# Kernel optimization log

Hardware: AMD Instinct MI355X
Metric: run time of the kernel (lower is better)

Reference implementation:

```python
import jax, jax.numpy as jnp
import numpy as np

B, S, H, GLU, VOC, L, CIN, BLK = 8, 256, 512, 1024, 256, 24, 320, 16
EPS = 1e-5


def setup_inputs() -> dict:
    key = jax.random.key(0)
    ks = jax.random.split(key, 16)
    r = lambda k, shp, s=0.02: (jax.random.normal(k, shp) * s).astype(jnp.float32)
    return {
        "x": jax.random.normal(ks[0], (B, CIN, 1, S), dtype=jnp.float32),
        "stem_w": r(ks[1], (H, CIN)),
        "rms_local": jnp.ones((L, H), jnp.float32),
        "rms_global": jnp.ones((L, H), jnp.float32),
        "rms_ffn": jnp.ones((L, H), jnp.float32),
        # alphas init to 0.0 in the torch module; use small nonzero values so
        # all sublayers actually contribute to the output / gradients.
        "alpha_local": (jax.random.normal(ks[2], (L,)) * 0.1).astype(jnp.float32),
        "alpha_global": (jax.random.normal(ks[3], (L,)) * 0.1).astype(jnp.float32),
        "alpha_mlp": (jax.random.normal(ks[4], (L,)) * 0.1).astype(jnp.float32),
        "w_local": r(ks[5], (L, H, BLK, BLK), 0.06),   # per-channel 16x16 mixing mats
        "w_global": r(ks[6], (L, H, BLK, BLK), 0.06),
        "wv": r(ks[7], (L, GLU, H)),
        "wg": r(ks[8], (L, GLU, H)),
        "wo": r(ks[9], (L, H, GLU)),
        "head_rms": jnp.ones((H,), jnp.float32),
        "head_logit_scale": jnp.float32(1.0),
        "head_w": r(ks[10], (VOC, H)),
    }


def _rmsnorm(h, w):
    # h: [B,C,S], w: [C]; mean-of-squares over channel axis (C == HIDDEN == 512)
    ms = jnp.mean(h * h, axis=1, keepdims=True)
    return h * jax.lax.rsqrt(ms + EPS) * w[None, :, None]


def _forward(x, stem_w, rms_local, rms_global, rms_ffn, alpha_local, alpha_global,
             alpha_mlp, w_local, w_global, wv, wg, wo, head_rms, head_logit_scale, head_w):
    h = jnp.einsum('oc,bcs->bos', stem_w, x[:, :, 0, :])  # stem conv1x1 -> [B,H,S]
    params = (rms_local, rms_global, rms_ffn, alpha_local, alpha_global, alpha_mlp,
              w_local, w_global, wv, wg, wo)

    def step(h, p):
        rl, rg, rf, al, ag, am, Wl, Wg, Wv, Wgt, Wo = p
        # s = i*16 + j : i = chunk index, j = within-chunk position
        u = _rmsnorm(h, rl).reshape(B, H, BLK, BLK)
        h = h + al * jnp.einsum('cpj,bcij->bcip', Wl, u).reshape(B, H, S)   # local: mix j
        v = _rmsnorm(h, rg).reshape(B, H, BLK, BLK)
        h = h + ag * jnp.einsum('cpi,bcij->bcpj', Wg, v).reshape(B, H, S)   # global: mix i
        w_ = _rmsnorm(h, rf)
        h1 = jnp.einsum('oc,bcs->bos', Wv, w_)
        h3 = jnp.einsum('oc,bcs->bos', Wgt, w_)
        h = h + am * jnp.einsum('co,bos->bcs', Wo, jax.nn.silu(h1) * h3)    # GLU MLP
        return h, None

    h, _ = jax.lax.scan(step, h, params)
    n = _rmsnorm(h, head_rms)
    logits = head_logit_scale * jnp.einsum('vc,bcs->bvs', head_w, n)
    return logits[:, :, None, :]  # [B, VOCAB, 1, S]


def reference(x, stem_w, rms_local, rms_global, rms_ffn, alpha_local, alpha_global,
              alpha_mlp, w_local, w_global, wv, wg, wo, head_rms, head_logit_scale, head_w):
    return _forward(x, stem_w, rms_local, rms_global, rms_ffn, alpha_local, alpha_global,
                    alpha_mlp, w_local, w_global, wv, wg, wo, head_rms,
                    head_logit_scale, head_w)
```

## Files before the change

kernel.cpp:

```cpp
#include <hip/hip_runtime.h>
#include <hip/hip_bf16.h>
#include <stdint.h>

#define NB 8
#define NS 256
#define NH 512
#define NG 1024
#define NV 256
#define NL 24
#define NC 320
#define NT 2048
#define EPSF 1e-5f

typedef __bf16 bf16;
typedef bf16 bf16x8 __attribute__((ext_vector_type(8)));
typedef float f32x4 __attribute__((ext_vector_type(4)));

__device__ __forceinline__ bf16 f2bf(float f) {
    uint32_t u = __builtin_bit_cast(uint32_t, f);
    u += 0x7FFFu + ((u >> 16) & 1u);
    uint16_t b = (uint16_t)(u >> 16);
    return __builtin_bit_cast(bf16, b);
}
__device__ __forceinline__ uint16_t bfbits(float f) {
    uint32_t u = __builtin_bit_cast(uint32_t, f);
    u += 0x7FFFu + ((u >> 16) & 1u);
    return (uint16_t)(u >> 16);
}

__device__ __forceinline__ void gload16(const void* g, void* l) {
    __builtin_amdgcn_global_load_lds(
        (const __attribute__((address_space(1))) void*)g,
        (__attribute__((address_space(3))) void*)l,
        16, 0, 0);
}

__device__ __forceinline__ void stage64(
    const bf16* __restrict__ src, int ldk, bf16* lds, int wv_, int lane)
{
    #pragma unroll
    for (int j = 0; j < 2; ++j) {
        const int gI = wv_*2 + j;
        const int r  = gI*8 + (lane >> 3);
        const int ch = (lane & 7) ^ (lane >> 3);
        gload16(src + (size_t)r*ldk + ch*8, lds + gI*512);
    }
}
__device__ __forceinline__ const bf16x8* fragp(const bf16* lds, int row, int ch) {
    return (const bf16x8*)(lds + row*64 + ((ch ^ (row & 7)) << 3));
}

#define MFMA(a,b,c) __builtin_amdgcn_mfma_f32_16x16x32_bf16(a, b, c, 0, 0, 0)

__global__ __launch_bounds__(256) void k_cvt(
    const float* __restrict__ src, bf16* __restrict__ dst, int n8)
{
    int i = blockIdx.x*256 + threadIdx.x;
    const int stride = gridDim.x*256;
    for (; i < n8; i += stride) {
        const float* sp = src + (size_t)i*8;
        float4 v0 = *(const float4*)&sp[0];
        float4 v1 = *(const float4*)&sp[4];
        bf16x8 t;
        t[0] = f2bf(v0.x); t[1] = f2bf(v0.y); t[2] = f2bf(v0.z); t[3] = f2bf(v0.w);
        t[4] = f2bf(v1.x); t[5] = f2bf(v1.y); t[6] = f2bf(v1.z); t[7] = f2bf(v1.w);
        *(bf16x8*)&dst[(size_t)i*8] = t;
    }
}

__global__ __launch_bounds__(256) void k_cvt2(
    const float* __restrict__ s0, const float* __restrict__ s1,
    bf16* __restrict__ d0, bf16* __restrict__ d1, int n8a, int n8b)
{
    const int N = n8a + n8b;
    for (int i = blockIdx.x*256 + threadIdx.x; i < N; i += gridDim.x*256) {
        const float* s; bf16* d; int j;
        if (i < n8a) { s = s0; d = d0; j = i; }
        else         { s = s1; d = d1; j = i - n8a; }
        const float* sp = s + (size_t)j*8;
        float4 v0 = *(const float4*)&sp[0];
        float4 v1 = *(const float4*)&sp[4];
        bf16x8 t;
        t[0] = f2bf(v0.x); t[1] = f2bf(v0.y); t[2] = f2bf(v0.z); t[3] = f2bf(v0.w);
        t[4] = f2bf(v1.x); t[5] = f2bf(v1.y); t[6] = f2bf(v1.z); t[7] = f2bf(v1.w);
        *(bf16x8*)&d[(size_t)j*8] = t;
    }
}

__global__ __launch_bounds__(256) void k_trw(
    const float* __restrict__ wl, const float* __restrict__ wg,
    bf16* __restrict__ wlT, bf16* __restrict__ wgT)
{
    __shared__ bf16 Ls[64*72];
    const int pj0 = blockIdx.x*64, c0 = blockIdx.y*64;
    const int z = blockIdx.z, l = z >> 1;
    const float* src = (z & 1) ? wg : wl;
    bf16* dst = (z & 1) ? wgT : wlT;
    src += (size_t)l*NH*256;
    dst += (size_t)l*256*NH;
    const int tid = threadIdx.x;
    #pragma unroll
    for (int e = 0; e < 16; ++e) {
        int idx = e*256 + tid;
        int cl = idx >> 6, pj = idx & 63;
        Ls[pj*72 + cl] = f2bf(src[(size_t)(c0 + cl)*256 + pj0 + pj]);
    }
    __syncthreads();
    #pragma unroll
    for (int e = 0; e < 2; ++e) {
        int idx = e*256 + tid;
        int row = idx >> 3, ch8 = idx & 7;
        *(bf16x8*)&dst[(size_t)(pj0 + row)*NH + c0 + ch8*8] =
            *(const bf16x8*)&Ls[row*72 + ch8*8];
    }
}

__global__ __launch_bounds__(256) void k_trx(
    const float* __restrict__ x, bf16* __restrict__ xT)
{
    __shared__ bf16 Ls[64*72];
    const int s0 = blockIdx.x*64, c0 = blockIdx.y*64, b = blockIdx.z;
    const int tid = threadIdx.x;
    #pragma unroll
    for (int e = 0; e < 16; ++e) {
        int idx = tid + e*256;
        int c = idx >> 6, s = idx & 63;
        Ls[s*72 + c] = f2bf(x[(size_t)(b*NC + c0 + c)*NS + s0 + s]);
    }
    __syncthreads();
    #pragma unroll
    for (int e = 0; e < 2; ++e) {
        int idx = tid + e*256;
        int s = idx >> 3, ch = idx & 7;
        *(bf16x8*)&xT[(size_t)(b*NS + s0 + s)*NC + c0 + ch*8] =
            *(const bf16x8*)&Ls[s*72 + ch*8];
    }
}

__global__ __launch_bounds__(256) void k_stem_b(
    const bf16* __restrict__ xT, const bf16* __restrict__ wb,
    float* __restrict__ h)
{
    __shared__ __align__(16) bf16 As[2][4096], Bs[2][4096];
    __shared__ float Cs[64*66];
    const int t0 = blockIdx.x*64, n0 = blockIdx.y*64;
    const int tid = threadIdx.x, lane = tid & 63, wv_ = tid >> 6;
    const int wm = wv_ >> 1, wn = wv_ & 1;
    const int fr = lane & 15, kq = lane >> 4;
    const bf16* Ag = xT + (size_t)t0*NC;
    const bf16* Bg = wb + (size_t)n0*NC;
    f32x4 acc[2][2] = {};
    stage64(Ag, NC, As[0], wv_, lane);
    stage64(Bg, NC, Bs[0], wv_, lane);
    __syncthreads();
    const int NIT = NC/64;
    for (int it = 0; it < NIT; ++it) {
        const int cur = it & 1;
        if (it + 1 < NIT) {
            stage64(Ag + (it+1)*64, NC, As[cur^1], wv_, lane);
            stage64(Bg + (it+1)*64, NC, Bs[cur^1], wv_, lane);
        }
        #pragma unroll
        for (int kk = 0; kk < 2; ++kk) {
            const int ch = kk*4 + kq;
            bf16x8 a0 = *fragp(As[cur], wm*32 + fr,      ch);
            bf16x8 a1 = *fragp(As[cur], wm*32 + 16 + fr, ch);
            bf16x8 b0 = *fragp(Bs[cur], wn*32 + fr,      ch);
            bf16x8 b1 = *fragp(Bs[cur], wn*32 + 16 + fr, ch);
            acc[0][0] = MFMA(a0, b0, acc[0][0]);
            acc[0][1] = MFMA(a0, b1, acc[0][1]);
            acc[1][0] = MFMA(a1, b0, acc[1][0]);
            acc[1][1] = MFMA(a1, b1, acc[1][1]);
        }
        __syncthreads();
    }
    const int row4 = (lane >> 4)*4, col = lane & 15;
    #pragma unroll
    for (int mi = 0; mi < 2; ++mi)
      #pragma unroll
      for (int ni = 0; ni < 2; ++ni)
        #pragma unroll
        for (int r = 0; r < 4; ++r)
            Cs[(wm*32 + mi*16 + row4 + r)*66 + wn*32 + ni*16 + col] = acc[mi][ni][r];
    __syncthreads();
    const int rr = tid >> 2, c16 = (tid & 3)*16;
    float* dst = &h[(size_t)(t0 + rr)*NH + n0 + c16];
    #pragma unroll
    for (int i = 0; i < 16; ++i) dst[i] = Cs[rr*66 + c16 + i];
}

template<int STR, bool FFN>
__global__ __launch_bounds__(256) void k_mix2(
    float* __restrict__ h, const bf16* __restrict__ wT,
    const float* __restrict__ rmsw, const float* __restrict__ alpha_p,
    const float* __restrict__ rmsw_ffn, bf16* __restrict__ a_bf)
{
    __shared__ float raw[16][512];
    __shared__ float red[4][16];
    __shared__ float rstdL[16];
    const int b = blockIdx.x, gi = blockIdx.y, ph = blockIdx.z;
    const int base = b*NS + (STR == 1 ? gi*16 : gi);
    const int tid = threadIdx.x, lane = tid & 63, wid = tid >> 6;
    #pragma unroll
    for (int e = 0; e < 8; ++e) {
        int idx = e*256 + tid;
        int k = idx >> 7, c4 = idx & 127;
        *(float4*)&raw[k][c4*4] = *(const float4*)&h[(size_t)(base + k*STR)*NH + c4*4];
    }
    __syncthreads();
    const int c0 = tid*2;
    float u0[16], u1[16], part[16];
    #pragma unroll
    for (int k = 0; k < 16; ++k) {
        float A = raw[k][c0], B = raw[k][c0+1];
        u0[k] = A; u1[k] = B; part[k] = A*A + B*B;
    }
    #pragma unroll
    for (int m = 1; m < 64; m <<= 1)
        #pragma unroll
        for (int k = 0; k < 16; ++k) part[k] += __shfl_xor(part[k], m, 64);
    if (lane == 0) {
        #pragma unroll
        for (int k = 0; k < 16; ++k) red[wid][k] = part[k];
    }
    __syncthreads();
    if (tid < 16)
        rstdL[tid] = rsqrtf((red[0][tid]+red[1][tid]+red[2][tid]+red[3][tid])*(1.f/NH) + EPSF);
    __syncthreads();
    #pragma unroll
    for (int k = 0; k < 16; ++k) { u0[k] *= rstdL[k]; u1[k] *= rstdL[k]; }
    const float al = *alpha_p;
    const float rc0 = rmsw[c0]*al, rc1 = rmsw[c0+1]*al;
    const uint32_t* wrow = (const uint32_t*)wT + tid;
    float hn0[8], hn1[8];
    #pragma unroll
    for (int pp = 0; pp < 8; ++pp) {
        const int p = ph*8 + pp;
        float a0 = 0.f, a1 = 0.f;
        #pragma unroll
        for (int k = 0; k < 16; ++k) {
            uint32_t wz = wrow[(p*16 + k)*256];
            float w0 = __builtin_bit_cast(float, wz << 16);
            float w1 = __builtin_bit_cast(float, wz & 0xffff0000u);
            a0 += w0*u0[k]; a1 += w1*u1[k];
        }
        hn0[pp] = raw[p][c0]   + rc0*a0;
        hn1[pp] = raw[p][c0+1] + rc1*a1;
        float2 o; o.x = hn0[pp]; o.y = hn1[pp];
        *(float2*)&h[(size_t)(base + p*STR)*NH + c0] = o;
    }
    if constexpr (FFN) {
        float p2[8];
        #pragma unroll
        for (int pp = 0; pp < 8; ++pp) p2[pp] = hn0[pp]*hn0[pp] + hn1[pp]*hn1[pp];
        #pragma unroll
        for (int m = 1; m < 64; m <<= 1)
            #pragma unroll
            for (int pp = 0; pp < 8; ++pp) p2[pp] += __shfl_xor(p2[pp], m, 64);
        __syncthreads();
        if (lane == 0) {
            #pragma unroll
            for (int pp = 0; pp < 8; ++pp) red[wid][pp] = p2[pp];
        }
        __syncthreads();
        if (tid < 8)
            rstdL[tid] = rsqrtf((red[0][tid]+red[1][tid]+red[2][tid]+red[3][tid])*(1.f/NH) + EPSF);
        __syncthreads();
        const float rf0 = rmsw_ffn[c0], rf1 = rmsw_ffn[c0+1];
        #pragma unroll
        for (int pp = 0; pp < 8; ++pp) {
            const int p = ph*8 + pp;
            float r = rstdL[pp];
            uint32_t pk = ((uint32_t)bfbits(hn1[pp]*r*rf1) << 16) | bfbits(hn0[pp]*r*rf0);
            *(uint32_t*)&a_bf[(size_t)(base + p*STR)*NH + c0] = pk;
        }
    }
}

__global__ __launch_bounds__(256) void k_norm2(
    const float* __restrict__ h, const float* __restrict__ rmsw,
    bf16* __restrict__ a)
{
    const int t = blockIdx.x*4 + (threadIdx.x >> 6);
    const int lane = threadIdx.x & 63;
    const int c8 = lane*8;
    const float* src = &h[(size_t)t*NH + c8];
    float4 h0 = *(const float4*)&src[0];
    float4 h1 = *(const float4*)&src[4];
    float ss = h0.x*h0.x + h0.y*h0.y + h0.z*h0.z + h0.w*h0.w
             + h1.x*h1.x + h1.y*h1.y + h1.z*h1.z + h1.w*h1.w;
    #pragma unroll
    for (int m = 1; m < 64; m <<= 1) ss += __shfl_xor(ss, m, 64);
    const float rstd = rsqrtf(ss*(1.f/NH) + EPSF);
    float4 w0 = *(const float4*)&rmsw[c8];
    float4 w1 = *(const float4*)&rmsw[c8 + 4];
    bf16x8 o;
    o[0] = f2bf(h0.x*rstd*w0.x); o[1] = f2bf(h0.y*rstd*w0.y);
    o[2] = f2bf(h0.z*rstd*w0.z); o[3] = f2bf(h0.w*rstd*w0.w);
    o[4] = f2bf(h1.x*rstd*w1.x); o[5] = f2bf(h1.y*rstd*w1.y);
    o[6] = f2bf(h1.z*rstd*w1.z); o[7] = f2bf(h1.w*rstd*w1.w);
    *(bf16x8*)&a[(size_t)t*NH + c8] = o;
}

__global__ __launch_bounds__(256) void k_mlp_in(
    const bf16* __restrict__ a, const bf16* __restrict__ wvl,
    const bf16* __restrict__ wgl, bf16* __restrict__ g)
{
    __shared__ __align__(16) char sm[65536];
    bf16* As  = (bf16*)sm;
    bf16* B1s = (bf16*)(sm + 32768);
    bf16* B3s = (bf16*)(sm + 49152);
    bf16* Gs  = (bf16*)sm;
    const int t0 = blockIdx.x*128, n0 = blockIdx.y*64;
    const int tid = threadIdx.x, lane = tid & 63, wv_ = tid >> 6;
    const int wm = wv_ >> 1, wn = wv_ & 1;
    const int fr = lane & 15, kq = lane >> 4;
    const bf16* Ag = a   + (size_t)t0*NH;
    const bf16* Vg = wvl + (size_t)n0*NH;
    const bf16* Gg = wgl + (size_t)n0*NH;
    f32x4 acc1[4][2] = {}, acc3[4][2] = {};
    stage64(Ag, NH, As, wv_, lane);
    stage64(Ag + (size_t)64*NH, NH, As + 4096, wv_, lane);
    stage64(Vg, NH, B1s, wv_, lane);
    stage64(Gg, NH, B3s, wv_, lane);
    __syncthreads();
    const int NIT = NH/64;
    for (int it = 0; it < NIT; ++it) {
        const int cur = it & 1;
        if (it + 1 < NIT) {
            const bf16* Ak = Ag + (it+1)*64;
            stage64(Ak, NH, As + (cur^1)*8192, wv_, lane);
            stage64(Ak + (size_t)64*NH, NH, As + (cur^1)*8192 + 4096, wv_, lane);
            stage64(Vg + (it+1)*64, NH, B1s + (cur^1)*4096, wv_, lane);
            stage64(Gg + (it+1)*64, NH, B3s + (cur^1)*4096, wv_, lane);
        }
        #pragma unroll
        for (int kk = 0; kk < 2; ++kk) {
            const int ch = kk*4 + kq;
            bf16x8 am[4];
            #pragma unroll
            for (int mi = 0; mi < 4; ++mi)
                am[mi] = *fragp(As + cur*8192, wm*64 + mi*16 + fr, ch);
            bf16x8 u0 = *fragp(B1s + cur*4096, wn*32 + fr,      ch);
            bf16x8 u1 = *fragp(B1s + cur*4096, wn*32 + 16 + fr, ch);
            bf16x8 v0 = *fragp(B3s + cur*4096, wn*32 + fr,      ch);
            bf16x8 v1 = *fragp(B3s + cur*4096, wn*32 + 16 + fr, ch);
            #pragma unroll
            for (int mi = 0; mi < 4; ++mi) {
                acc1[mi][0] = MFMA(am[mi], u0, acc1[mi][0]);
                acc1[mi][1] = MFMA(am[mi], u1, acc1[mi][1]);
                acc3[mi][0] = MFMA(am[mi], v0, acc3[mi][0]);
                acc3[mi][1] = MFMA(am[mi], v1, acc3[mi][1]);
            }
        }
        __syncthreads();
    }
    const int row4 = (lane >> 4)*4, col = lane & 15;
    #pragma unroll
    for (int mi = 0; mi < 4; ++mi)
      #pragma unroll
      for (int ni = 0; ni < 2; ++ni)
        #pragma unroll
        for (int r = 0; r < 4; ++r) {
            float xv = acc1[mi][ni][r];
            float gl = (xv / (1.f + __expf(-xv))) * acc3[mi][ni][r];
            Gs[(wm*64 + mi*16 + row4 + r)*72 + wn*32 + ni*16 + col] = f2bf(gl);
        }
    __syncthreads();
    const int rr = tid >> 1, c32 = (tid & 1)*32;
    #pragma unroll
    for (int j = 0; j < 4; ++j)
        *(bf16x8*)&g[(size_t)(t0 + rr)*NG + n0 + c32 + j*8] =
            *(const bf16x8*)&Gs[rr*72 + c32 + j*8];
}

__global__ __launch_bounds__(256) void k_mlp_out(
    const bf16* __restrict__ g, const bf16* __restrict__ wol,
    const float* __restrict__ alpha_p, float* __restrict__ h)
{
    __shared__ __align__(16) char sm[49152];
    bf16* As = (bf16*)sm;
    bf16* Bs = (bf16*)(sm + 32768);
    float* Cs = (float*)sm;
    const int t0 = blockIdx.x*128, n0 = blockIdx.y*64;
    const int tid = threadIdx.x, lane = tid & 63, wv_ = tid >> 6;
    const int wm = wv_ >> 1, wn = wv_ & 1;
    const int fr = lane & 15, kq = lane >> 4;
    const bf16* Ag = g   + (size_t)t0*NG;
    const bf16* Bg = wol + (size_t)n0*NG;
    f32x4 acc[4][2] = {};
    stage64(Ag, NG, As, wv_, lane);
    stage64(Ag + (size_t)64*NG, NG, As + 4096, wv_, lane);
    stage64(Bg, NG, Bs, wv_, lane);
    __syncthreads();
    const int NIT = NG/64;
    for (int it = 0; it < NIT; ++it) {
        const int cur = it & 1;
        if (it + 1 < NIT) {
            const bf16* Ak = Ag + (it+1)*64;
            stage64(Ak, NG, As + (cur^1)*8192, wv_, lane);
            stage64(Ak + (size_t)64*NG, NG, As + (cur^1)*8192 + 4096, wv_, lane);
            stage64(Bg + (it+1)*64, NG, Bs + (cur^1)*4096, wv_, lane);
        }
        #pragma unroll
        for (int kk = 0; kk < 2; ++kk) {
            const int ch = kk*4 + kq;
            bf16x8 am[4];
            #pragma unroll
            for (int mi = 0; mi < 4; ++mi)
                am[mi] = *fragp(As + cur*8192, wm*64 + mi*16 + fr, ch);
            bf16x8 b0 = *fragp(Bs + cur*4096, wn*32 + fr,      ch);
            bf16x8 b1 = *fragp(Bs + cur*4096, wn*32 + 16 + fr, ch);
            #pragma unroll
            for (int mi = 0; mi < 4; ++mi) {
                acc[mi][0] = MFMA(am[mi], b0, acc[mi][0]);
                acc[mi][1] = MFMA(am[mi], b1, acc[mi][1]);
            }
        }
        __syncthreads();
    }
    const int row4 = (lane >> 4)*4, col = lane & 15;
    #pragma unroll
    for (int mi = 0; mi < 4; ++mi)
      #pragma unroll
      for (int ni = 0; ni < 2; ++ni)
        #pragma unroll
        for (int r = 0; r < 4; ++r)
            Cs[(wm*64 + mi*16 + row4 + r)*66 + wn*32 + ni*16 + col] = acc[mi][ni][r];
    __syncthreads();
    const float am_ = *alpha_p;
    const int rr = tid >> 1, c32 = (tid & 1)*32;
    float* dst = &h[(size_t)(t0 + rr)*NH + n0 + c32];
    #pragma unroll
    for (int j = 0; j < 8; ++j) {
        float4 hv = *(const float4*)&dst[j*4];
        float4 cv = *(const float4*)&Cs[rr*66 + c32 + j*4];
        hv.x += am_*cv.x; hv.y += am_*cv.y; hv.z += am_*cv.z; hv.w += am_*cv.w;
        *(float4*)&dst[j*4] = hv;
    }
}

__global__ __launch_bounds__(256) void k_head(
    const bf16* __restrict__ a, const bf16* __restrict__ hw,
    const float* __restrict__ scale_p, float* __restrict__ out)
{
    __shared__ __align__(16) bf16 As[2][4096], Bs[2][4096];
    __shared__ float Ls[64*66];
    const int t0 = blockIdx.x*64, n0 = blockIdx.y*64;
    const int tid = threadIdx.x, lane = tid & 63, wv_ = tid >> 6;
    const int wm = wv_ >> 1, wn = wv_ & 1;
    const int fr = lane & 15, kq = lane >> 4;
    const bf16* Ag = a  + (size_t)t0*NH;
    const bf16* Bg = hw + (size_t)n0*NH;
    f32x4 acc[2][2] = {};
    stage64(Ag, NH, As[0], wv_, lane);
    stage64(Bg, NH, Bs[0], wv_, lane);
    __syncthreads();
    const int NIT = NH/64;
    for (int it = 0; it < NIT; ++it) {
        const int cur = it & 1;
        if (it + 1 < NIT) {
            stage64(Ag + (it+1)*64, NH, As[cur^1], wv_, lane);
            stage64(Bg + (it+1)*64, NH, Bs[cur^1], wv_, lane);
        }
        #pragma unroll
        for (int kk = 0; kk < 2; ++kk) {
            const int ch = kk*4 + kq;
            bf16x8 a0 = *fragp(As[cur], wm*32 + fr,      ch);
            bf16x8 a1 = *fragp(As[cur], wm*32 + 16 + fr, ch);
            bf16x8 b0 = *fragp(Bs[cur], wn*32 + fr,      ch);
            bf16x8 b1 = *fragp(Bs[cur], wn*32 + 16 + fr, ch);
            acc[0][0] = MFMA(a0, b0, acc[0][0]);
            acc[0][1] = MFMA(a0, b1, acc[0][1]);
            acc[1][0] = MFMA(a1, b0, acc[1][0]);
            acc[1][1] = MFMA(a1, b1, acc[1][1]);
        }
        __syncthreads();
    }
    const float sc = *scale_p;
    const int row4 = (lane >> 4)*4, col = lane & 15;
    #pragma unroll
    for (int mi = 0; mi < 2; ++mi)
      #pragma unroll
      for (int ni = 0; ni < 2; ++ni)
        #pragma unroll
        for (int r = 0; r < 4; ++r)
            Ls[(wm*32 + mi*16 + row4 + r)*66 + wn*32 + ni*16 + col] = sc * acc[mi][ni][r];
    __syncthreads();
    const int vv = tid >> 2, s16 = (tid & 3)*16;
    const int b = t0 >> 8, s0 = t0 & 255;
    float* dst = &out[((size_t)(b*NV + n0 + vv))*NS + s0 + s16];
    #pragma unroll
    for (int i = 0; i < 16; ++i) dst[i] = Ls[(s16 + i)*66 + vv];
}

extern "C" void kernel_launch(void* const* d_in, const int* in_sizes, int n_in,
                              void* d_out, int out_size, void* d_ws, size_t ws_size,
                              hipStream_t stream) {
    const float* x          = (const float*)d_in[0];
    const float* stem_w     = (const float*)d_in[1];
    const float* rms_local  = (const float*)d_in[2];
    const float* rms_global = (const float*)d_in[3];
    const float* rms_ffn    = (const float*)d_in[4];
    const float* alpha_local  = (const float*)d_in[5];
    const float* alpha_global = (const float*)d_in[6];
    const float* alpha_mlp    = (const float*)d_in[7];
    const float* w_local    = (const float*)d_in[8];
    const float* w_global   = (const float*)d_in[9];
    const float* wv         = (const float*)d_in[10];
    const float* wg         = (const float*)d_in[11];
    const float* wo         = (const float*)d_in[12];
    const float* head_rms   = (const float*)d_in[13];
    const float* head_scale = (const float*)d_in[14];
    const float* head_w     = (const float*)d_in[15];
    float* out = (float*)d_out;

    char* ws = (char*)d_ws;
    const size_t MB = 1024*1024;
    float* h    = (float*)(ws);
    bf16*  g    = (bf16*)(ws + 4*MB);
    bf16*  a_bf = (bf16*)(ws + 8*MB);
    bf16* xT      = (bf16*)(ws + 16*MB);
    bf16* stem_wb = (bf16*)(ws + 18*MB);
    bf16* head_wb = (bf16*)(ws + 19*MB);
    bf16* wlT     = (bf16*)(ws + 20*MB);
    bf16* wgT     = (bf16*)(ws + 26*MB);
    bf16* wv_b    = (bf16*)(ws + 32*MB);
    bf16* wg_b    = (bf16*)(ws + 56*MB);
    bf16* wo_b    = (bf16*)(ws + 80*MB);

    k_cvt<<<2048, 256, 0, stream>>>(wv, wv_b, NL*NG*NH/8);
    k_cvt<<<2048, 256, 0, stream>>>(wg, wg_b, NL*NG*NH/8);
    k_cvt<<<2048, 256, 0, stream>>>(wo, wo_b, NL*NH*NG/8);
    k_cvt2<<<160, 256, 0, stream>>>(stem_w, head_w, stem_wb, head_wb,
                                    NH*NC/8, NV*NH/8);
    k_trw<<<dim3(4, 8, 48), 256, 0, stream>>>(w_local, w_global, wlT, wgT);
    k_trx<<<dim3(4, 5, 8), 256, 0, stream>>>(x, xT);

    k_stem_b<<<dim3(32, 8), 256, 0, stream>>>(xT, stem_wb, h);

    for (int l = 0; l < NL; ++l) {
        k_mix2<1, false><<<dim3(NB, 16, 2), 256, 0, stream>>>(
            h, wlT + (size_t)l*256*NH, rms_local + l*NH, alpha_local + l,
            nullptr, nullptr);
        k_mix2<16, true><<<dim3(NB, 16, 2), 256, 0, stream>>>(
            h, wgT + (size_t)l*256*NH, rms_global + l*NH, alpha_global + l,
            rms_ffn + l*NH, a_bf);
        k_mlp_in<<<dim3(16, 16), 256, 0, stream>>>(
            a_bf, wv_b + (size_t)l*NG*NH, wg_b + (size_t)l*NG*NH, g);
        k_mlp_out<<<dim3(16, 8), 256, 0, stream>>>(
            g, wo_b + (size_t)l*NH*NG, alpha_mlp + l, h);
    }
    k_norm2<<<512, 256, 0, stream>>>(h, head_rms, a_bf);
    k_head<<<dim3(32, 4), 256, 0, stream>>>(a_bf, head_wb, head_scale, out);
}
```

Baseline: 1.138 ms.

## Merge weight conversions into one kernel and shrink mlp_out tiles to double grid

The three per-matrix fp32-to-bf16 conversion launches and the stem/head conversion are merged into a single grid-stride kernel, removing three launches. The MLP output GEMM tile shrinks from 128x64 to 64x64 rows per block, so the grid grows from 128 to 256 blocks and covers more of the GPU's compute units. Each block now does fewer MFMAs per LDS load, so data reuse drops and the weight tile is streamed more times.

```diff
diff --git a/kernel.cpp b/kernel.cpp
--- a/kernel.cpp
+++ b/kernel.cpp
@@ -52,31 +52,24 @@
 
 #define MFMA(a,b,c) __builtin_amdgcn_mfma_f32_16x16x32_bf16(a, b, c, 0, 0, 0)
 
-__global__ __launch_bounds__(256) void k_cvt(
-    const float* __restrict__ src, bf16* __restrict__ dst, int n8)
-{
-    int i = blockIdx.x*256 + threadIdx.x;
-    const int stride = gridDim.x*256;
-    for (; i < n8; i += stride) {
-        const float* sp = src + (size_t)i*8;
-        float4 v0 = *(const float4*)&sp[0];
-        float4 v1 = *(const float4*)&sp[4];
-        bf16x8 t;
-        t[0] = f2bf(v0.x); t[1] = f2bf(v0.y); t[2] = f2bf(v0.z); t[3] = f2bf(v0.w);
-        t[4] = f2bf(v1.x); t[5] = f2bf(v1.y); t[6] = f2bf(v1.z); t[7] = f2bf(v1.w);
-        *(bf16x8*)&dst[(size_t)i*8] = t;
-    }
-}
-
-__global__ __launch_bounds__(256) void k_cvt2(
-    const float* __restrict__ s0, const float* __restrict__ s1,
-    bf16* __restrict__ d0, bf16* __restrict__ d1, int n8a, int n8b)
-{
-    const int N = n8a + n8b;
+__global__ __launch_bounds__(256) void k_cvt_all(
+    const float* __restrict__ wv, const float* __restrict__ wg,
+    const float* __restrict__ wo, const float* __restrict__ sw,
+    const float* __restrict__ hw, bf16* __restrict__ dwv,
+    bf16* __restrict__ dwg, bf16* __restrict__ dwo,
+    bf16* __restrict__ dsw, bf16* __restrict__ dhw)
+{
+    const int n1 = NL*NG*NH/8;
+    const int n4 = NH*NC/8;
+    const int n5 = NV*NH/8;
+    const int N = 3*n1 + n4 + n5;
     for (int i = blockIdx.x*256 + threadIdx.x; i < N; i += gridDim.x*256) {
         const float* s; bf16* d; int j;
-        if (i < n8a) { s = s0; d = d0; j = i; }
-        else         { s = s1; d = d1; j = i - n8a; }
+        if (i < n1)            { s = wv; d = dwv; j = i; }
+        else if (i < 2*n1)     { s = wg; d = dwg; j = i - n1; }
+        else if (i < 3*n1)     { s = wo; d = dwo; j = i - 2*n1; }
+        else if (i < 3*n1+n4)  { s = sw; d = dsw; j = i - 3*n1; }
+        else                   { s = hw; d = dhw; j = i - 3*n1 - n4; }
         const float* sp = s + (size_t)j*8;
         float4 v0 = *(const float4*)&sp[0];
         float4 v1 = *(const float4*)&sp[4];
@@ -378,65 +371,57 @@
     const bf16* __restrict__ g, const bf16* __restrict__ wol,
     const float* __restrict__ alpha_p, float* __restrict__ h)
 {
-    __shared__ __align__(16) char sm[49152];
-    bf16* As = (bf16*)sm;
-    bf16* Bs = (bf16*)(sm + 32768);
-    float* Cs = (float*)sm;
-    const int t0 = blockIdx.x*128, n0 = blockIdx.y*64;
+    __shared__ __align__(16) bf16 As[2][4096], Bs[2][4096];
+    __shared__ float Cs[64*66];
+    const int t0 = blockIdx.x*64, n0 = blockIdx.y*64;
     const int tid = threadIdx.x, lane = tid & 63, wv_ = tid >> 6;
     const int wm = wv_ >> 1, wn = wv_ & 1;
     const int fr = lane & 15, kq = lane >> 4;
     const bf16* Ag = g   + (size_t)t0*NG;
     const bf16* Bg = wol + (size_t)n0*NG;
-    f32x4 acc[4][2] = {};
-    stage64(Ag, NG, As, wv_, lane);
-    stage64(Ag + (size_t)64*NG, NG, As + 4096, wv_, lane);
-    stage64(Bg, NG, Bs, wv_, lane);
+    f32x4 acc[2][2] = {};
+    stage64(Ag, NG, As[0], wv_, lane);
+    stage64(Bg, NG, Bs[0], wv_, lane);
     __syncthreads();
     const int NIT = NG/64;
     for (int it = 0; it < NIT; ++it) {
         const int cur = it & 1;
         if (it + 1 < NIT) {
-            const bf16* Ak = Ag + (it+1)*64;
-            stage64(Ak, NG, As + (cur^1)*8192, wv_, lane);
-            stage64(Ak + (size_t)64*NG, NG, As + (cur^1)*8192 + 4096, wv_, lane);
-            stage64(Bg + (it+1)*64, NG, Bs + (cur^1)*4096, wv_, lane);
+            stage64(Ag + (it+1)*64, NG, As[cur^1], wv_, lane);
+            stage64(Bg + (it+1)*64, NG, Bs[cur^1], wv_, lane);
         }
         #pragma unroll
         for (int kk = 0; kk < 2; ++kk) {
             const int ch = kk*4 + kq;
-            bf16x8 am[4];
-            #pragma unroll
-            for (int mi = 0; mi < 4; ++mi)
-                am[mi] = *fragp(As + cur*8192, wm*64 + mi*16 + fr, ch);
-            bf16x8 b0 = *fragp(Bs + cur*4096, wn*32 + fr,      ch);
-            bf16x8 b1 = *fragp(Bs + cur*4096, wn*32 + 16 + fr, ch);
-            #pragma unroll
-            for (int mi = 0; mi < 4; ++mi) {
-                acc[mi][0] = MFMA(am[mi], b0, acc[mi][0]);
-                acc[mi][1] = MFMA(am[mi], b1, acc[mi][1]);
-            }
+            bf16x8 a0 = *fragp(As[cur], wm*32 + fr,      ch);
+            bf16x8 a1 = *fragp(As[cur], wm*32 + 16 + fr, ch);
+            bf16x8 b0 = *fragp(Bs[cur], wn*32 + fr,      ch);
+            bf16x8 b1 = *fragp(Bs[cur], wn*32 + 16 + fr, ch);
+            acc[0][0] = MFMA(a0, b0, acc[0][0]);
+            acc[0][1] = MFMA(a0, b1, acc[0][1]);
+            acc[1][0] = MFMA(a1, b0, acc[1][0]);
+            acc[1][1] = MFMA(a1, b1, acc[1][1]);
         }
         __syncthreads();
     }
     const int row4 = (lane >> 4)*4, col = lane & 15;
     #pragma unroll
-    for (int mi = 0; mi < 4; ++mi)
+    for (int mi = 0; mi < 2; ++mi)
       #pragma unroll
       for (int ni = 0; ni < 2; ++ni)
         #pragma unroll
         for (int r = 0; r < 4; ++r)
-            Cs[(wm*64 + mi*16 + row4 + r)*66 + wn*32 + ni*16 + col] = acc[mi][ni][r];
-    __syncthreads();
-    const float am_ = *alpha_p;
-    const int rr = tid >> 1, c32 = (tid & 1)*32;
-    float* dst = &h[(size_t)(t0 + rr)*NH + n0 + c32];
-    #pragma unroll
-    for (int j = 0; j < 8; ++j) {
-        float4 hv = *(const float4*)&dst[j*4];
-        float4 cv = *(const float4*)&Cs[rr*66 + c32 + j*4];
-        hv.x += am_*cv.x; hv.y += am_*cv.y; hv.z += am_*cv.z; hv.w += am_*cv.w;
-        *(float4*)&dst[j*4] = hv;
+            Cs[(wm*32 + mi*16 + row4 + r)*66 + wn*32 + ni*16 + col] = acc[mi][ni][r];
+    __syncthreads();
+    const float am = *alpha_p;
+    const int rr = tid >> 2, c16 = (tid & 3)*16;
+    float* dst = &h[(size_t)(t0 + rr)*NH + n0 + c16];
+    #pragma unroll
+    for (int i = 0; i < 4; ++i) {
+        float4 hv = *(const float4*)&dst[i*4];
+        float4 cv = *(const float4*)&Cs[rr*66 + c16 + i*4];
+        hv.x += am*cv.x; hv.y += am*cv.y; hv.z += am*cv.z; hv.w += am*cv.w;
+        *(float4*)&dst[i*4] = hv;
     }
 }
 
@@ -529,11 +514,8 @@
     bf16* wg_b    = (bf16*)(ws + 56*MB);
     bf16* wo_b    = (bf16*)(ws + 80*MB);
 
-    k_cvt<<<2048, 256, 0, stream>>>(wv, wv_b, NL*NG*NH/8);
-    k_cvt<<<2048, 256, 0, stream>>>(wg, wg_b, NL*NG*NH/8);
-    k_cvt<<<2048, 256, 0, stream>>>(wo, wo_b, NL*NH*NG/8);
-    k_cvt2<<<160, 256, 0, stream>>>(stem_w, head_w, stem_wb, head_wb,
-                                    NH*NC/8, NV*NH/8);
+    k_cvt_all<<<4096, 256, 0, stream>>>(wv, wg, wo, stem_w, head_w,
+                                        wv_b, wg_b, wo_b, stem_wb, head_wb);
     k_trw<<<dim3(4, 8, 48), 256, 0, stream>>>(w_local, w_global, wlT, wgT);
     k_trx<<<dim3(4, 5, 8), 256, 0, stream>>>(x, xT);
 
@@ -548,7 +530,7 @@
             rms_ffn + l*NH, a_bf);
         k_mlp_in<<<dim3(16, 16), 256, 0, stream>>>(
             a_bf, wv_b + (size_t)l*NG*NH, wg_b + (size_t)l*NG*NH, g);
-        k_mlp_out<<<dim3(16, 8), 256, 0, stream>>>(
+        k_mlp_out<<<dim3(32, 8), 256, 0, stream>>>(
             g, wo_b + (size_t)l*NH*NG, alpha_mlp + l, h);
     }
     k_norm2<<<512, 256, 0, stream>>>(h, head_rms, a_bf);
```

Result: slower. 1.192 ms (+4.7%).
